# Kernel optimization log

Hardware: AMD Instinct MI355X
Metric: run time of the kernel (lower is better)

The kernel has to match this reference:

```python
import jax, jax.numpy as jnp
import numpy as np

N, E, D, H, C, HOPS = 50000, 1600000, 128, 4, 32, 3

def spectral_normalize(W, iters=5):
    # power iteration, fixed start vector (deterministic, jit-friendly)
    u = jnp.ones((W.shape[0],), W.dtype) / jnp.sqrt(jnp.float32(W.shape[0]))
    for _ in range(iters):
        v = W.T @ u; v = v / (jnp.linalg.norm(v) + 1e-12)
        u = W @ v;  u = u / (jnp.linalg.norm(u) + 1e-12)
    sigma = u @ (W @ v)
    return W / (sigma + 1e-12)

def layer_norm(x, g, b, eps=1e-5):
    m = jnp.mean(x, -1, keepdims=True)
    v = jnp.mean((x - m) ** 2, -1, keepdims=True)
    return (x - m) * jax.lax.rsqrt(v + eps) * g + b

def edge_softmax(logits, dst):
    # logits: [E, H]; softmax over edges sharing a destination node
    m = jax.ops.segment_max(logits, dst, num_segments=N)
    e = jnp.exp(logits - m[dst])
    s = jax.ops.segment_sum(e, dst, num_segments=N)
    return e / (s[dst] + 1e-16)

def gat_layer(h, src, dst, W, a_s, a_d, bias):
    xh = (h @ W).reshape(N, H, C)                      # [N,H,C]
    al_s = jnp.sum(xh * a_s, -1)                       # [N,H]
    al_d = jnp.sum(xh * a_d, -1)
    logits = jax.nn.leaky_relu(al_s[src] + al_d[dst], 0.2)  # [E,H]
    alpha = edge_softmax(logits, dst)                  # [E,H]
    msg = xh[src] * alpha[..., None]                   # [E,H,C]
    out = jax.ops.segment_sum(msg, dst, num_segments=N)
    return out.reshape(N, H * C) + bias

def ode_block(h, W_ode, b_ode, steps=4):
    # fixed-step RK4 over t in [0,1]; f(h) = gelu(h @ sn(W) + b)
    Wn = spectral_normalize(W_ode)
    f = lambda y: jax.nn.gelu(y @ Wn + b_ode, approximate=False)
    dt = 1.0 / steps
    def step(y, _):
        k1 = f(y); k2 = f(y + 0.5 * dt * k1)
        k3 = f(y + 0.5 * dt * k2); k4 = f(y + dt * k3)
        return y + (dt / 6.0) * (k1 + 2 * k2 + 2 * k3 + k4), None
    y, _ = jax.lax.scan(step, h, None, length=steps)
    return y

def multihop_broadcast(h, src, dst, att):
    deg = jnp.maximum(jax.ops.segment_sum(jnp.ones((E,), h.dtype), dst, num_segments=N), 1.0)
    hops = [h]
    cur = h
    for _ in range(HOPS):
        cur = jax.ops.segment_sum(cur[src], dst, num_segments=N) / deg[:, None]
        hops.append(cur)
    stack = jnp.stack(hops)                            # [HOPS+1, N, D]
    scores = jnp.einsum('knd,d->kn', stack, att)       # [HOPS+1, N]
    w = jax.nn.softmax(scores, axis=0)
    return jnp.einsum('kn,knd->nd', w, stack)

def encoder_fwd(x, edge_index, W_in, b_in, W1, a_src1, a_dst1, b1,
                W2, a_src2, a_dst2, b2, g1, be1, g2, be2, W_ode, b_ode, att):
    src, dst = edge_index[0], edge_index[1]
    h = jax.nn.gelu(x @ spectral_normalize(W_in) + b_in, approximate=False)
    h = layer_norm(jax.nn.gelu(gat_layer(h, src, dst, W1, a_src1, a_dst1, b1), approximate=False), g1, be1)
    h = layer_norm(jax.nn.gelu(gat_layer(h, src, dst, W2, a_src2, a_dst2, b2), approximate=False), g2, be2)
    h = ode_block(h, W_ode, b_ode)
    h = multihop_broadcast(h, src, dst, att)
    return h

def setup_inputs() -> dict:
    key = jax.random.key(0)
    ks = jax.random.split(key, 12)
    s = lambda d: 1.0 / np.sqrt(d)
    return {
        'x': jax.random.normal(ks[0], (N, D), jnp.float32),
        'edge_index': jax.random.randint(ks[1], (2, E), 0, N, jnp.int64),
        'W_in': jax.random.normal(ks[2], (D, D), jnp.float32) * s(D),
        'b_in': jnp.zeros((D,), jnp.float32),
        'W1': jax.random.normal(ks[3], (D, H * C), jnp.float32) * s(D),
        'a_src1': jax.random.normal(ks[4], (H, C), jnp.float32) * s(C),
        'a_dst1': jax.random.normal(ks[5], (H, C), jnp.float32) * s(C),
        'b1': jnp.zeros((H * C,), jnp.float32),
        'W2': jax.random.normal(ks[6], (D, H * C), jnp.float32) * s(D),
        'a_src2': jax.random.normal(ks[7], (H, C), jnp.float32) * s(C),
        'a_dst2': jax.random.normal(ks[8], (H, C), jnp.float32) * s(C),
        'b2': jnp.zeros((H * C,), jnp.float32),
        'g1': jnp.ones((D,), jnp.float32), 'be1': jnp.zeros((D,), jnp.float32),
        'g2': jnp.ones((D,), jnp.float32), 'be2': jnp.zeros((D,), jnp.float32),
        'W_ode': jax.random.normal(ks[9], (D, D), jnp.float32) * s(D),
        'b_ode': jnp.zeros((D,), jnp.float32),
        'att': jax.random.normal(ks[10], (D,), jnp.float32) * s(D),
    }

def reference(x, edge_index, W_in, b_in, W1, a_src1, a_dst1, b1, W2, a_src2, a_dst2, b2,
              g1, be1, g2, be2, W_ode, b_ode, att):
    return encoder_fwd(x, edge_index, W_in, b_in, W1, a_src1, a_dst1, b1,
                       W2, a_src2, a_dst2, b2, g1, be1, g2, be2, W_ode, b_ode, att)
```

## Files before the change

kernel.cpp:

```cpp
#include <hip/hip_runtime.h>
#include <math.h>


typedef __attribute__((ext_vector_type(8))) short bf16x8;
typedef __attribute__((ext_vector_type(4))) float f32x4;

__device__ __forceinline__ float gelu_f(float x) {
    return 0.5f * x * (1.0f + erff(x * 0.70710678118654752f));
}
__device__ __forceinline__ unsigned pack_bf16(float a, float b) {
    unsigned ua = __float_as_uint(a), ub = __float_as_uint(b);
    ua += 0x7fffu + ((ua >> 16) & 1u);
    ub += 0x7fffu + ((ub >> 16) & 1u);
    return (ua >> 16) | (ub & 0xffff0000u);
}
__device__ __forceinline__ unsigned short bfbits(float x) {
    unsigned u = __float_as_uint(x);
    u += 0x7fffu + ((u >> 16) & 1u);
    return (unsigned short)(u >> 16);
}
__device__ __forceinline__ float bf_lo(unsigned u) { return __uint_as_float(u << 16); }
__device__ __forceinline__ float bf_hi(unsigned u) { return __uint_as_float(u & 0xffff0000u); }
__device__ __forceinline__ int swz(int byte) { return byte ^ (((byte >> 8) & 15) << 4); }

__launch_bounds__(128, 1)
__global__ void sn_k(const float* __restrict__ Win, const float* __restrict__ Wode,
                     float* __restrict__ WnIn, float* __restrict__ WnOde)
{
    __shared__ float Ws[128 * 128];
    __shared__ float Wt[128 * 128];
    __shared__ float red[128];
    const float* W  = (blockIdx.x == 0) ? Win  : Wode;
    float*       Wn = (blockIdx.x == 0) ? WnIn : WnOde;
    const int t = threadIdx.x;

    for (int i = t * 4; i < 16384; i += 512) {
        float4 v = *(const float4*)&W[i];
        *(float4*)&Ws[i] = v;
        int r = i >> 7, c = i & 127;
        Wt[(c + 0) * 128 + r] = v.x;
        Wt[(c + 1) * 128 + r] = v.y;
        Wt[(c + 2) * 128 + r] = v.z;
        Wt[(c + 3) * 128 + r] = v.w;
    }
    __syncthreads();

    float u = 0.088388347648318447f;
    float v = 0.0f;
    for (int it = 0; it < 5; it++) {
        red[t] = u; __syncthreads();
        float vv = 0.f;
        for (int i = 0; i < 128; i++) vv = fmaf(Ws[i * 128 + t], red[i], vv);
        __syncthreads();
        red[t] = vv * vv; __syncthreads();
        for (int s = 64; s > 0; s >>= 1) { if (t < s) red[t] += red[t + s]; __syncthreads(); }
        float nv = sqrtf(red[0]) + 1e-12f;
        v = vv / nv;
        __syncthreads();
        red[t] = v; __syncthreads();
        float uu = 0.f;
        for (int i = 0; i < 128; i++) uu = fmaf(Wt[i * 128 + t], red[i], uu);
        __syncthreads();
        red[t] = uu * uu; __syncthreads();
        for (int s = 64; s > 0; s >>= 1) { if (t < s) red[t] += red[t + s]; __syncthreads(); }
        float nu = sqrtf(red[0]) + 1e-12f;
        u = uu / nu;
        __syncthreads();
    }
    red[t] = v; __syncthreads();
    float wv = 0.f;
    for (int i = 0; i < 128; i++) wv = fmaf(Wt[i * 128 + t], red[i], wv);
    __syncthreads();
    red[t] = u * wv; __syncthreads();
    for (int s = 64; s > 0; s >>= 1) { if (t < s) red[t] += red[t + s]; __syncthreads(); }
    float inv = 1.0f / (red[0] + 1e-12f);
    __syncthreads();
    for (int i = t * 4; i < 16384; i += 512) {
        float4 w = *(const float4*)&Ws[i];
        w.x *= inv; w.y *= inv; w.z *= inv; w.w *= inv;
        *(float4*)&Wn[i] = w;
    }
}

__global__ void hist_k(const int* __restrict__ dst, int* __restrict__ deg, int E, int N)
{
    int e = blockIdx.x * blockDim.x + threadIdx.x;
    if (e < E) {
        int d = dst[e];
        d = (d < 0) ? 0 : (d >= N ? N - 1 : d);
        atomicAdd(&deg[d], 1);
    }
}

__launch_bounds__(1024, 1)
__global__ void scan_k(const int* __restrict__ deg, int* __restrict__ offs, int n)
{
    __shared__ int part[1024];
    const int t = threadIdx.x;
    const int chunk = (n + 1023) >> 10;
    int lo = t * chunk; if (lo > n) lo = n;
    int hi = lo + chunk; if (hi > n) hi = n;
    int s = 0;
    for (int i = lo; i < hi; i++) s += deg[i];
    part[t] = s; __syncthreads();
    for (int d = 1; d < 1024; d <<= 1) {
        int v = (t >= d) ? part[t - d] : 0;
        __syncthreads();
        part[t] += v;
        __syncthreads();
    }
    int run = (t == 0) ? 0 : part[t - 1];
    for (int i = lo; i < hi; i++) { offs[i] = run; run += deg[i]; }
    if (t == 1023) offs[n] = run;
}

__global__ void scatter_k(const int* __restrict__ src, const int* __restrict__ dst,
                          const int* __restrict__ offs, int* __restrict__ cursor,
                          int* __restrict__ col, int E, int N)
{
    int e = blockIdx.x * blockDim.x + threadIdx.x;
    if (e < E) {
        int d = dst[e];
        d = (d < 0) ? 0 : (d >= N ? N - 1 : d);
        int s = src[e];
        s = (s < 0) ? 0 : (s >= N ? N - 1 : s);
        int pos = offs[d] + atomicAdd(&cursor[d], 1);
        col[pos] = s;
    }
}

__launch_bounds__(256, 2)
__global__ void gemm128_k(const float* __restrict__ in, const float* __restrict__ W,
                          const float* __restrict__ bias, float* __restrict__ out_f32,
                          unsigned* __restrict__ out_bf, int nrows, int mode,
                          const float* __restrict__ a_s, const float* __restrict__ a_d,
                          float* __restrict__ als, float* __restrict__ ald)
{
    __shared__ float Ws[128 * 128];
    const int t = threadIdx.x;
    const int n0 = blockIdx.x * 128;

    for (int i = t * 4; i < 16384; i += 1024)
        *(float4*)&Ws[i] = *(const float4*)&W[i];
    __syncthreads();

    const int cg = t & 15, rg = t >> 4;
    const int c0 = cg * 8, r0 = rg * 8;

    const float* xrow[8];
    bool rowok[8];
#pragma unroll
    for (int i = 0; i < 8; i++) {
        int r = n0 + r0 + i;
        rowok[i] = (r < nrows);
        int rc = rowok[i] ? r : (nrows - 1);
        xrow[i] = in + (size_t)rc * 128;
    }

    float acc[8][8];
#pragma unroll
    for (int i = 0; i < 8; i++)
#pragma unroll
        for (int j = 0; j < 8; j++) acc[i][j] = 0.f;

    for (int k = 0; k < 128; k += 4) {
        float4 xv[8];
#pragma unroll
        for (int i = 0; i < 8; i++) xv[i] = *(const float4*)(xrow[i] + k);
#pragma unroll
        for (int kk = 0; kk < 4; kk++) {
            float4 w0 = *(const float4*)&Ws[(k + kk) * 128 + c0];
            float4 w1 = *(const float4*)&Ws[(k + kk) * 128 + c0 + 4];
#pragma unroll
            for (int i = 0; i < 8; i++) {
                float xk = (kk == 0) ? xv[i].x : (kk == 1) ? xv[i].y : (kk == 2) ? xv[i].z : xv[i].w;
                acc[i][0] = fmaf(xk, w0.x, acc[i][0]);
                acc[i][1] = fmaf(xk, w0.y, acc[i][1]);
                acc[i][2] = fmaf(xk, w0.z, acc[i][2]);
                acc[i][3] = fmaf(xk, w0.w, acc[i][3]);
                acc[i][4] = fmaf(xk, w1.x, acc[i][4]);
                acc[i][5] = fmaf(xk, w1.y, acc[i][5]);
                acc[i][6] = fmaf(xk, w1.z, acc[i][6]);
                acc[i][7] = fmaf(xk, w1.w, acc[i][7]);
            }
        }
    }

    if (mode == 0) {
        const int h = cg >> 2, coff = (cg & 3) * 8;
        float ps[8], pd[8];
#pragma unroll
        for (int i = 0; i < 8; i++) {
            float s_ = 0.f, d_ = 0.f;
#pragma unroll
            for (int j = 0; j < 8; j++) {
                s_ = fmaf(acc[i][j], a_s[h * 32 + coff + j], s_);
                d_ = fmaf(acc[i][j], a_d[h * 32 + coff + j], d_);
            }
            ps[i] = s_; pd[i] = d_;
        }
#pragma unroll
        for (int mk = 1; mk < 4; mk <<= 1) {
#pragma unroll
            for (int i = 0; i < 8; i++) {
                ps[i] += __shfl_xor(ps[i], mk);
                pd[i] += __shfl_xor(pd[i], mk);
            }
        }
        if ((cg & 3) == 0) {
#pragma unroll
            for (int i = 0; i < 8; i++) if (rowok[i]) {
                als[(size_t)(n0 + r0 + i) * 4 + h] = ps[i];
                ald[(size_t)(n0 + r0 + i) * 4 + h] = pd[i];
            }
        }
#pragma unroll
        for (int i = 0; i < 8; i++) if (rowok[i]) {
            size_t b = (size_t)(n0 + r0 + i) * 64 + cg * 4;
            uint4 o;
            o.x = pack_bf16(acc[i][0], acc[i][1]);
            o.y = pack_bf16(acc[i][2], acc[i][3]);
            o.z = pack_bf16(acc[i][4], acc[i][5]);
            o.w = pack_bf16(acc[i][6], acc[i][7]);
            *(uint4*)&out_bf[b] = o;
        }
    } else {
#pragma unroll
        for (int i = 0; i < 8; i++) if (rowok[i]) {
            size_t b = (size_t)(n0 + r0 + i) * 128 + c0;
            float o[8];
#pragma unroll
            for (int j = 0; j < 8; j++) o[j] = gelu_f(acc[i][j] + bias[c0 + j]);
            *(float4*)&out_f32[b]     = make_float4(o[0], o[1], o[2], o[3]);
            *(float4*)&out_f32[b + 4] = make_float4(o[4], o[5], o[6], o[7]);
        }
    }
}

__launch_bounds__(256)
__global__ void gat_agg2_k(const unsigned* __restrict__ xhbf, const float* __restrict__ als,
                           const float* __restrict__ ald, const int* __restrict__ col,
                           const int* __restrict__ offs, const float* __restrict__ bias,
                           const float* __restrict__ g, const float* __restrict__ be,
                           float* __restrict__ hout, int nnodes)
{
    __shared__ float alph[4][64][4];
    __shared__ int   scol[4][64];
    const int w = threadIdx.x >> 6;
    const int n = blockIdx.x * 4 + w;
    if (n >= nnodes) return;
    const int lane = threadIdx.x & 63;
    const int e0 = offs[n], e1 = offs[n + 1];
    const float4 aldv = *(const float4*)&ald[(size_t)n * 4];

    float m0 = -1e30f, m1 = -1e30f, m2 = -1e30f, m3 = -1e30f;
    float s0 = 0.f, s1 = 0.f, s2 = 0.f, s3 = 0.f;
    for (int i = e0 + lane; i < e1; i += 64) {
        int sv = col[i];
        float4 av = *(const float4*)&als[(size_t)sv * 4];
        float l0 = av.x + aldv.x; l0 = l0 > 0.f ? l0 : 0.2f * l0;
        float l1 = av.y + aldv.y; l1 = l1 > 0.f ? l1 : 0.2f * l1;
        float l2 = av.z + aldv.z; l2 = l2 > 0.f ? l2 : 0.2f * l2;
        float l3 = av.w + aldv.w; l3 = l3 > 0.f ? l3 : 0.2f * l3;
        float M;
        M = fmaxf(m0, l0); s0 = s0 * __expf(m0 - M) + __expf(l0 - M); m0 = M;
        M = fmaxf(m1, l1); s1 = s1 * __expf(m1 - M) + __expf(l1 - M); m1 = M;
        M = fmaxf(m2, l2); s2 = s2 * __expf(m2 - M) + __expf(l2 - M); m2 = M;
        M = fmaxf(m3, l3); s3 = s3 * __expf(m3 - M) + __expf(l3 - M); m3 = M;
    }
#pragma unroll
    for (int mk = 1; mk < 64; mk <<= 1) {
        float mo, so, M;
        mo = __shfl_xor(m0, mk); so = __shfl_xor(s0, mk);
        M = fmaxf(m0, mo); s0 = s0 * __expf(m0 - M) + so * __expf(mo - M); m0 = M;
        mo = __shfl_xor(m1, mk); so = __shfl_xor(s1, mk);
        M = fmaxf(m1, mo); s1 = s1 * __expf(m1 - M) + so * __expf(mo - M); m1 = M;
        mo = __shfl_xor(m2, mk); so = __shfl_xor(s2, mk);
        M = fmaxf(m2, mo); s2 = s2 * __expf(m2 - M) + so * __expf(mo - M); m2 = M;
        mo = __shfl_xor(m3, mk); so = __shfl_xor(s3, mk);
        M = fmaxf(m3, mo); s3 = s3 * __expf(m3 - M) + so * __expf(mo - M); m3 = M;
    }
    const float i0 = 1.f / (s0 + 1e-16f), i1 = 1.f / (s1 + 1e-16f);
    const float i2 = 1.f / (s2 + 1e-16f), i3 = 1.f / (s3 + 1e-16f);

    const int hh = lane >> 4;
    float ax = 0.f, ay = 0.f;
    for (int base = e0; base < e1; base += 64) {
        int idx = base + lane;
        if (idx < e1) {
            int sv = col[idx];
            float4 av = *(const float4*)&als[(size_t)sv * 4];
            float l0 = av.x + aldv.x; l0 = l0 > 0.f ? l0 : 0.2f * l0;
            float l1 = av.y + aldv.y; l1 = l1 > 0.f ? l1 : 0.2f * l1;
            float l2 = av.z + aldv.z; l2 = l2 > 0.f ? l2 : 0.2f * l2;
            float l3 = av.w + aldv.w; l3 = l3 > 0.f ? l3 : 0.2f * l3;
            float4 a4;
            a4.x = __expf(l0 - m0) * i0;
            a4.y = __expf(l1 - m1) * i1;
            a4.z = __expf(l2 - m2) * i2;
            a4.w = __expf(l3 - m3) * i3;
            *(float4*)&alph[w][lane][0] = a4;
            scol[w][lane] = sv;
        }
        int cnt = e1 - base; if (cnt > 64) cnt = 64;
#pragma unroll 4
        for (int j = 0; j < cnt; j++) {
            int sj = scol[w][j];
            float aj = alph[w][j][hh];
            unsigned u = xhbf[(size_t)sj * 64 + lane];
            ax = fmaf(aj, bf_lo(u), ax);
            ay = fmaf(aj, bf_hi(u), ay);
        }
    }

    const int c0 = lane * 2;
    float v0 = gelu_f(ax + bias[c0]);
    float v1 = gelu_f(ay + bias[c0 + 1]);
    float sum = v0 + v1;
#pragma unroll
    for (int mk = 32; mk >= 1; mk >>= 1) sum += __shfl_xor(sum, mk);
    float mean = sum * (1.0f / 128.0f);
    float d0 = v0 - mean, d1 = v1 - mean;
    float vs = d0 * d0 + d1 * d1;
#pragma unroll
    for (int mk = 32; mk >= 1; mk >>= 1) vs += __shfl_xor(vs, mk);
    float rstd = rsqrtf(vs * (1.0f / 128.0f) + 1e-5f);
    size_t b = (size_t)n * 128 + c0;
    hout[b]     = d0 * rstd * g[c0] + be[c0];
    hout[b + 1] = d1 * rstd * g[c0 + 1] + be[c0 + 1];
}

__launch_bounds__(256, 4)
__global__ void ode_mfma_k(const float* __restrict__ yin, const float* __restrict__ Wn,
                           const float* __restrict__ bias, unsigned short* __restrict__ ybf,
                           int nrows, int nchunks)
{
    __shared__ unsigned short Wt[128 * 128];
    __shared__ unsigned short tl[2][16 * 128];
    const int t = threadIdx.x;
    const int w = t >> 6, lane = t & 63;
    const int pair = w >> 1, hf = w & 1;
    const int cl = lane & 15, lg = lane >> 4;

    for (int i = t; i < 16384; i += 256) {
        int k = i >> 7, c = i & 127;
        *(unsigned short*)((char*)Wt + swz((c << 8) + (k << 1))) = bfbits(Wn[i]);
    }

    float bcol[4];
#pragma unroll
    for (int n = 0; n < 4; n++) bcol[n] = bias[(hf * 4 + n) * 16 + cl];

    const float dt = 0.25f;
    char* tbase = (char*)&tl[pair][0];

    int chunk = blockIdx.x * 2 + pair;
    if (chunk > nchunks - 1) chunk = nchunks - 1;
    const int r0 = chunk * 16;

    for (int i2 = hf * 64 + lane; i2 < 512; i2 += 128) {
        int r = i2 >> 5, k0 = (i2 & 31) * 4;
        int rc = r0 + r; if (rc > nrows - 1) rc = nrows - 1;
        float4 v = *(const float4*)&yin[(size_t)rc * 128 + k0];
        *(uint2*)(tbase + swz(r * 256 + k0 * 2)) =
            make_uint2(pack_bf16(v.x, v.y), pack_bf16(v.z, v.w));
    }
    float yv[4][4], av[4][4];
#pragma unroll
    for (int q = 0; q < 4; q++) {
        int rc = r0 + lg * 4 + q; if (rc > nrows - 1) rc = nrows - 1;
        const float* rp = &yin[(size_t)rc * 128 + hf * 64 + cl];
#pragma unroll
        for (int n = 0; n < 4; n++) { yv[n][q] = rp[n * 16]; av[n][q] = yv[n][q]; }
    }
    __syncthreads();

#pragma unroll 1
    for (int step = 0; step < 4; step++) {
#pragma unroll 1
        for (int st = 0; st < 4; st++) {
            const float ca = (st == 0 || st == 3) ? dt / 6.f : dt / 3.f;
            const float ct = (st < 2) ? dt * 0.5f : dt;
            const bool last = (st == 3);
            bf16x8 af[4];
#pragma unroll
            for (int ks = 0; ks < 4; ks++)
                af[ks] = *(const bf16x8*)(tbase + swz(cl * 256 + ks * 64 + lg * 16));
            f32x4 acc[4];
#pragma unroll
            for (int n = 0; n < 4; n++) {
                acc[n] = (f32x4){0.f, 0.f, 0.f, 0.f};
#pragma unroll
                for (int ks = 0; ks < 4; ks++) {
                    bf16x8 bf = *(const bf16x8*)((char*)Wt +
                                  swz(((hf * 4 + n) * 16 + cl) * 256 + ks * 64 + lg * 16));
                    acc[n] = __builtin_amdgcn_mfma_f32_16x16x32_bf16(af[ks], bf, acc[n], 0, 0, 0);
                }
            }
            __syncthreads();
#pragma unroll
            for (int n = 0; n < 4; n++) {
#pragma unroll
                for (int q = 0; q < 4; q++) {
                    float kk = gelu_f(acc[n][q] + bcol[n]);
                    av[n][q] = fmaf(ca, kk, av[n][q]);
                    float tn;
                    if (last) { yv[n][q] = av[n][q]; tn = av[n][q]; }
                    else      { tn = fmaf(ct, kk, yv[n][q]); }
                    int rr = lg * 4 + q;
                    *(unsigned short*)(tbase +
                        swz(rr * 256 + ((hf * 4 + n) * 16 + cl) * 2)) = bfbits(tn);
                }
            }
            __syncthreads();
        }
    }
#pragma unroll
    for (int q = 0; q < 4; q++) {
        int rg = r0 + lg * 4 + q;
        if (rg < nrows) {
#pragma unroll
            for (int n = 0; n < 4; n++)
                ybf[(size_t)rg * 128 + hf * 64 + n * 16 + cl] = bfbits(av[n][q]);
        }
    }
}

__launch_bounds__(256)
__global__ void hop_k(const unsigned* __restrict__ cur, const int* __restrict__ col,
                      const int* __restrict__ offs, const int* __restrict__ deg,
                      unsigned* __restrict__ outbf, int nnodes)
{
    __shared__ int scol[4][64];
    const int w = threadIdx.x >> 6;
    const int n = blockIdx.x * 4 + w;
    if (n >= nnodes) return;
    const int lane = threadIdx.x & 63;
    const int e0 = offs[n], e1 = offs[n + 1];
    float ax = 0.f, ay = 0.f;
    for (int base = e0; base < e1; base += 64) {
        int idx = base + lane;
        if (idx < e1) scol[w][lane] = col[idx];
        int cnt = e1 - base; if (cnt > 64) cnt = 64;
#pragma unroll 4
        for (int j = 0; j < cnt; j++) {
            int sj = scol[w][j];
            unsigned u = cur[(size_t)sj * 64 + lane];
            ax += bf_lo(u); ay += bf_hi(u);
        }
    }
    float dg = fmaxf((float)deg[n], 1.0f);
    outbf[(size_t)n * 64 + lane] = pack_bf16(ax / dg, ay / dg);
}

__launch_bounds__(256)
__global__ void final2_k(const unsigned* __restrict__ s0b, const unsigned* __restrict__ s1b,
                         const unsigned* __restrict__ s2b, const unsigned* __restrict__ s3b,
                         const float* __restrict__ att, float* __restrict__ outp, int nnodes)
{
    const int n = blockIdx.x * 4 + (threadIdx.x >> 6);
    if (n >= nnodes) return;
    const int lane = threadIdx.x & 63;
    size_t b = (size_t)n * 64 + lane;
    float2 a = *(const float2*)&att[lane * 2];
    unsigned u0 = s0b[b], u1 = s1b[b], u2 = s2b[b], u3 = s3b[b];
    float p0 = bf_lo(u0) * a.x + bf_hi(u0) * a.y;
    float p1 = bf_lo(u1) * a.x + bf_hi(u1) * a.y;
    float p2 = bf_lo(u2) * a.x + bf_hi(u2) * a.y;
    float p3 = bf_lo(u3) * a.x + bf_hi(u3) * a.y;
#pragma unroll
    for (int mk = 32; mk >= 1; mk >>= 1) {
        p0 += __shfl_xor(p0, mk); p1 += __shfl_xor(p1, mk);
        p2 += __shfl_xor(p2, mk); p3 += __shfl_xor(p3, mk);
    }
    float mm = fmaxf(fmaxf(p0, p1), fmaxf(p2, p3));
    float e0 = __expf(p0 - mm), e1 = __expf(p1 - mm), e2 = __expf(p2 - mm), e3 = __expf(p3 - mm);
    float inv = 1.0f / (e0 + e1 + e2 + e3);
    float w0 = e0 * inv, w1 = e1 * inv, w2 = e2 * inv, w3 = e3 * inv;
    float ox = w0 * bf_lo(u0) + w1 * bf_lo(u1) + w2 * bf_lo(u2) + w3 * bf_lo(u3);
    float oy = w0 * bf_hi(u0) + w1 * bf_hi(u1) + w2 * bf_hi(u2) + w3 * bf_hi(u3);
    *(float2*)&outp[(size_t)n * 128 + lane * 2] = make_float2(ox, oy);
}

extern "C" void kernel_launch(void* const* d_in, const int* in_sizes, int n_in,
                              void* d_out, int out_size, void* d_ws, size_t ws_size,
                              hipStream_t stream)
{
    const float* x     = (const float*)d_in[0];
    const int*   ei    = (const int*)d_in[1];
    const float* W_in  = (const float*)d_in[2];
    const float* b_in  = (const float*)d_in[3];
    const float* W1    = (const float*)d_in[4];
    const float* a_s1  = (const float*)d_in[5];
    const float* a_d1  = (const float*)d_in[6];
    const float* b1    = (const float*)d_in[7];
    const float* W2    = (const float*)d_in[8];
    const float* a_s2  = (const float*)d_in[9];
    const float* a_d2  = (const float*)d_in[10];
    const float* b2    = (const float*)d_in[11];
    const float* g1    = (const float*)d_in[12];
    const float* be1   = (const float*)d_in[13];
    const float* g2    = (const float*)d_in[14];
    const float* be2   = (const float*)d_in[15];
    const float* W_ode = (const float*)d_in[16];
    const float* b_ode = (const float*)d_in[17];
    const float* att   = (const float*)d_in[18];

    const int N = in_sizes[0] / 128;
    const int E = in_sizes[1] / 2;
    const int* srcv = ei;
    const int* dstv = ei + E;

    char* wsb = (char*)d_ws;
    size_t off = 0;
    auto alloc = [&](size_t bytes) -> void* {
        void* p = wsb + off;
        off = (off + bytes + 511) & ~(size_t)511;
        return p;
    };
    float*    WnIn   = (float*)alloc(65536);
    float*    WnOde  = (float*)alloc(65536);
    float*    als    = (float*)alloc((size_t)N * 4 * 4);
    float*    ald    = (float*)alloc((size_t)N * 4 * 4);
    int*      deg    = (int*)alloc((size_t)N * 4);
    int*      cursor = (int*)alloc((size_t)N * 4);
    int*      offs   = (int*)alloc((size_t)(N + 1) * 4);
    int*      col    = (int*)alloc((size_t)E * 4);
    float*    B0     = (float*)alloc((size_t)N * 128 * 4);
    unsigned* xhbf   = (unsigned*)alloc((size_t)N * 64 * 4);
    unsigned* ybf    = (unsigned*)alloc((size_t)N * 64 * 4);
    unsigned* h2bf   = (unsigned*)alloc((size_t)N * 64 * 4);
    unsigned* h3bf   = (unsigned*)alloc((size_t)N * 64 * 4);

    (void)hipMemsetAsync(deg, 0, (size_t)N * 4, stream);
    (void)hipMemsetAsync(cursor, 0, (size_t)N * 4, stream);

    sn_k<<<2, 128, 0, stream>>>(W_in, W_ode, WnIn, WnOde);
    hist_k<<<(E + 255) / 256, 256, 0, stream>>>(dstv, deg, E, N);
    scan_k<<<1, 1024, 0, stream>>>(deg, offs, N);
    scatter_k<<<(E + 255) / 256, 256, 0, stream>>>(srcv, dstv, offs, cursor, col, E, N);

    const int gblocks = (N + 127) / 128;
    const int ablocks = (N + 3) / 4;

    gemm128_k<<<gblocks, 256, 0, stream>>>(x, WnIn, b_in, B0, nullptr, N, 1,
        nullptr, nullptr, nullptr, nullptr);

    gemm128_k<<<gblocks, 256, 0, stream>>>(B0, W1, nullptr, nullptr, xhbf, N, 0,
        a_s1, a_d1, als, ald);
    gat_agg2_k<<<ablocks, 256, 0, stream>>>(xhbf, als, ald, col, offs, b1, g1, be1, B0, N);

    gemm128_k<<<gblocks, 256, 0, stream>>>(B0, W2, nullptr, nullptr, xhbf, N, 0,
        a_s2, a_d2, als, ald);
    gat_agg2_k<<<ablocks, 256, 0, stream>>>(xhbf, als, ald, col, offs, b2, g2, be2, B0, N);

    const int nchunks = (N + 15) / 16;
    const int oblocks = (nchunks + 1) / 2;
    ode_mfma_k<<<oblocks, 256, 0, stream>>>(B0, WnOde, b_ode, (unsigned short*)ybf, N, nchunks);

    hop_k<<<ablocks, 256, 0, stream>>>(ybf,  col, offs, deg, xhbf, N);
    hop_k<<<ablocks, 256, 0, stream>>>(xhbf, col, offs, deg, h2bf, N);
    hop_k<<<ablocks, 256, 0, stream>>>(h2bf, col, offs, deg, h3bf, N);
    final2_k<<<ablocks, 256, 0, stream>>>(ybf, xhbf, h2bf, h3bf, att, (float*)d_out, N);
}
```

Before: 787.2 us.

## Use bf16 MFMA for dense GEMMs and two-pass bucketed CSR scatter

Replaces the fp32 FMA register-tiled GEMM with a bf16 MFMA kernel that stages the input tile and the transposed weights in swizzled LDS, keeping the attention-logit reduction and gelu epilogues. It also replaces the per-edge global-atomic CSR scatter with a two-pass scheme: edges are first bucketed by 256-node destination ranges through LDS into a pair buffer, then each bucket is placed with LDS atomics. The aim is to cut ALU time in the GEMMs and global atomic contention in CSR construction. The cost is lower precision for the fp32 input and hidden activations (now rounded to bf16 before the GEMM), an extra kernel launch, and reuse of the ybf buffer as scratch space. Output stores in the MFMA GEMM are 2-byte scalar writes and may coalesce less well than the previous vector stores.

```diff
diff --git a/kernel.cpp b/kernel.cpp
--- a/kernel.cpp
+++ b/kernel.cpp
@@ -4,6 +4,8 @@
 
 typedef __attribute__((ext_vector_type(8))) short bf16x8;
 typedef __attribute__((ext_vector_type(4))) float f32x4;
+
+#define BSN 256
 
 __device__ __forceinline__ float gelu_f(float x) {
     return 0.5f * x * (1.0f + erff(x * 0.70710678118654752f));
@@ -114,126 +116,201 @@
     if (t == 1023) offs[n] = run;
 }
 
-__global__ void scatter_k(const int* __restrict__ src, const int* __restrict__ dst,
-                          const int* __restrict__ offs, int* __restrict__ cursor,
-                          int* __restrict__ col, int E, int N)
-{
-    int e = blockIdx.x * blockDim.x + threadIdx.x;
-    if (e < E) {
-        int d = dst[e];
-        d = (d < 0) ? 0 : (d >= N ? N - 1 : d);
-        int s = src[e];
-        s = (s < 0) ? 0 : (s >= N ? N - 1 : s);
-        int pos = offs[d] + atomicAdd(&cursor[d], 1);
-        col[pos] = s;
+__global__ void binit_k(const int* __restrict__ offs, int* __restrict__ bcur, int N, int nb)
+{
+    int b = blockIdx.x * blockDim.x + threadIdx.x;
+    if (b < nb) {
+        int n = b * BSN; if (n > N) n = N;
+        bcur[b] = offs[n];
     }
 }
 
 __launch_bounds__(256, 2)
-__global__ void gemm128_k(const float* __restrict__ in, const float* __restrict__ W,
-                          const float* __restrict__ bias, float* __restrict__ out_f32,
-                          unsigned* __restrict__ out_bf, int nrows, int mode,
-                          const float* __restrict__ a_s, const float* __restrict__ a_d,
-                          float* __restrict__ als, float* __restrict__ ald)
-{
-    __shared__ float Ws[128 * 128];
+__global__ void scatA_k(const int* __restrict__ src, const int* __restrict__ dst,
+                        int* __restrict__ bcur, uint2* __restrict__ pairbuf, int E, int N)
+{
+    __shared__ int cnt[256];
+    __shared__ int sc[256];
+    __shared__ int ebase[256];
+    __shared__ int delta[256];
+    __shared__ uint2 pr[4096];
+    __shared__ unsigned char bid[4096];
     const int t = threadIdx.x;
-    const int n0 = blockIdx.x * 128;
-
-    for (int i = t * 4; i < 16384; i += 1024)
-        *(float4*)&Ws[i] = *(const float4*)&W[i];
-    __syncthreads();
-
-    const int cg = t & 15, rg = t >> 4;
-    const int c0 = cg * 8, r0 = rg * 8;
-
-    const float* xrow[8];
-    bool rowok[8];
-#pragma unroll
-    for (int i = 0; i < 8; i++) {
-        int r = n0 + r0 + i;
-        rowok[i] = (r < nrows);
-        int rc = rowok[i] ? r : (nrows - 1);
-        xrow[i] = in + (size_t)rc * 128;
-    }
-
-    float acc[8][8];
-#pragma unroll
-    for (int i = 0; i < 8; i++)
-#pragma unroll
-        for (int j = 0; j < 8; j++) acc[i][j] = 0.f;
-
-    for (int k = 0; k < 128; k += 4) {
-        float4 xv[8];
-#pragma unroll
-        for (int i = 0; i < 8; i++) xv[i] = *(const float4*)(xrow[i] + k);
-#pragma unroll
-        for (int kk = 0; kk < 4; kk++) {
-            float4 w0 = *(const float4*)&Ws[(k + kk) * 128 + c0];
-            float4 w1 = *(const float4*)&Ws[(k + kk) * 128 + c0 + 4];
-#pragma unroll
-            for (int i = 0; i < 8; i++) {
-                float xk = (kk == 0) ? xv[i].x : (kk == 1) ? xv[i].y : (kk == 2) ? xv[i].z : xv[i].w;
-                acc[i][0] = fmaf(xk, w0.x, acc[i][0]);
-                acc[i][1] = fmaf(xk, w0.y, acc[i][1]);
-                acc[i][2] = fmaf(xk, w0.z, acc[i][2]);
-                acc[i][3] = fmaf(xk, w0.w, acc[i][3]);
-                acc[i][4] = fmaf(xk, w1.x, acc[i][4]);
-                acc[i][5] = fmaf(xk, w1.y, acc[i][5]);
-                acc[i][6] = fmaf(xk, w1.z, acc[i][6]);
-                acc[i][7] = fmaf(xk, w1.w, acc[i][7]);
+    const int e0 = blockIdx.x * 4096;
+
+    int s[16], d[16], rk[16], bb[16];
+    cnt[t] = 0;
+    __syncthreads();
+#pragma unroll
+    for (int i = 0; i < 16; i++) {
+        int e = e0 + i * 256 + t;
+        if (e < E) {
+            int dd = dst[e]; dd = (dd < 0) ? 0 : (dd >= N ? N - 1 : dd);
+            int ss = src[e]; ss = (ss < 0) ? 0 : (ss >= N ? N - 1 : ss);
+            s[i] = ss; d[i] = dd; bb[i] = dd >> 8;
+            rk[i] = atomicAdd(&cnt[bb[i]], 1);
+        } else bb[i] = -1;
+    }
+    __syncthreads();
+    sc[t] = cnt[t]; __syncthreads();
+    for (int st = 1; st < 256; st <<= 1) {
+        int v = (t >= st) ? sc[t - st] : 0;
+        __syncthreads();
+        sc[t] += v;
+        __syncthreads();
+    }
+    int excl = sc[t] - cnt[t];
+    int gbase = (cnt[t] > 0) ? atomicAdd(&bcur[t], cnt[t]) : 0;
+    ebase[t] = excl;
+    delta[t] = gbase - excl;
+    __syncthreads();
+#pragma unroll
+    for (int i = 0; i < 16; i++) {
+        if (bb[i] >= 0) {
+            int slot = ebase[bb[i]] + rk[i];
+            pr[slot] = make_uint2((unsigned)s[i], (unsigned)d[i]);
+            bid[slot] = (unsigned char)bb[i];
+        }
+    }
+    __syncthreads();
+    const int total = sc[255];
+    for (int i2 = t; i2 < total; i2 += 256) {
+        int b = bid[i2];
+        pairbuf[delta[b] + i2] = pr[i2];
+    }
+}
+
+__launch_bounds__(256, 4)
+__global__ void scatB_k(const uint2* __restrict__ pairbuf, const int* __restrict__ offs,
+                        int* __restrict__ col, int N)
+{
+    __shared__ int cur[BSN];
+    const int b = blockIdx.x;
+    const int n0 = b * BSN;
+    const int t = threadIdx.x;
+    int nn = N - n0; if (nn > BSN) nn = BSN;
+    if (t < nn) cur[t] = offs[n0 + t];
+    __syncthreads();
+    const int es = offs[n0], ee = offs[n0 + nn];
+    for (int e = es + t; e < ee; e += 256) {
+        uint2 p = pairbuf[e];
+        int pos = atomicAdd(&cur[(int)p.y - n0], 1);
+        col[pos] = (int)p.x;
+    }
+}
+
+__launch_bounds__(256, 2)
+__global__ void gemm_mfma_k(const float* __restrict__ in, const float* __restrict__ W,
+                            const float* __restrict__ bias, float* __restrict__ out_f32,
+                            unsigned short* __restrict__ out_bf, int nrows, int mode,
+                            const float* __restrict__ a_s, const float* __restrict__ a_d,
+                            float* __restrict__ als, float* __restrict__ ald)
+{
+    __shared__ unsigned short Wt[128 * 128];
+    __shared__ unsigned short As[128 * 128];
+    const int t = threadIdx.x;
+    const int w = t >> 6, lane = t & 63;
+    const int cl = lane & 15, lg = lane >> 4;
+    const int r0 = blockIdx.x * 128;
+
+    for (int i = t; i < 16384; i += 256) {
+        int k = i >> 7, c = i & 127;
+        *(unsigned short*)((char*)Wt + swz((c << 8) + (k << 1))) = bfbits(W[i]);
+    }
+    for (int i2 = t; i2 < 4096; i2 += 256) {
+        int r = i2 >> 5, k0 = (i2 & 31) * 4;
+        int rc = r0 + r; if (rc > nrows - 1) rc = nrows - 1;
+        float4 v = *(const float4*)&in[(size_t)rc * 128 + k0];
+        *(uint2*)((char*)As + swz((r << 8) + (k0 << 1))) =
+            make_uint2(pack_bf16(v.x, v.y), pack_bf16(v.z, v.w));
+    }
+    __syncthreads();
+
+    bf16x8 af[2][4];
+#pragma unroll
+    for (int rt = 0; rt < 2; rt++)
+#pragma unroll
+        for (int ks = 0; ks < 4; ks++)
+            af[rt][ks] = *(const bf16x8*)((char*)As +
+                           swz((w * 32 + rt * 16 + cl) * 256 + ks * 64 + lg * 16));
+
+    f32x4 acc[2][8];
+#pragma unroll
+    for (int rt = 0; rt < 2; rt++)
+#pragma unroll
+        for (int n = 0; n < 8; n++) acc[rt][n] = (f32x4){0.f, 0.f, 0.f, 0.f};
+
+#pragma unroll
+    for (int n = 0; n < 8; n++) {
+#pragma unroll
+        for (int ks = 0; ks < 4; ks++) {
+            bf16x8 bf = *(const bf16x8*)((char*)Wt +
+                          swz((n * 16 + cl) * 256 + ks * 64 + lg * 16));
+            acc[0][n] = __builtin_amdgcn_mfma_f32_16x16x32_bf16(af[0][ks], bf, acc[0][n], 0, 0, 0);
+            acc[1][n] = __builtin_amdgcn_mfma_f32_16x16x32_bf16(af[1][ks], bf, acc[1][n], 0, 0, 0);
+        }
+    }
+
+    if (mode == 0) {
+        float asv[4][2], adv[4][2];
+#pragma unroll
+        for (int h = 0; h < 4; h++) {
+            asv[h][0] = a_s[h * 32 + cl];      asv[h][1] = a_s[h * 32 + 16 + cl];
+            adv[h][0] = a_d[h * 32 + cl];      adv[h][1] = a_d[h * 32 + 16 + cl];
+        }
+#pragma unroll
+        for (int rt = 0; rt < 2; rt++) {
+#pragma unroll
+            for (int q = 0; q < 4; q++) {
+                int row = r0 + w * 32 + rt * 16 + lg * 4 + q;
+                float sh[4], dh[4];
+#pragma unroll
+                for (int h = 0; h < 4; h++) {
+                    sh[h] = acc[rt][2 * h][q] * asv[h][0] + acc[rt][2 * h + 1][q] * asv[h][1];
+                    dh[h] = acc[rt][2 * h][q] * adv[h][0] + acc[rt][2 * h + 1][q] * adv[h][1];
+                }
+#pragma unroll
+                for (int mk = 1; mk < 16; mk <<= 1) {
+#pragma unroll
+                    for (int h = 0; h < 4; h++) {
+                        sh[h] += __shfl_xor(sh[h], mk);
+                        dh[h] += __shfl_xor(dh[h], mk);
+                    }
+                }
+                if (cl == 0 && row < nrows) {
+#pragma unroll
+                    for (int h = 0; h < 4; h++) {
+                        als[(size_t)row * 4 + h] = sh[h];
+                        ald[(size_t)row * 4 + h] = dh[h];
+                    }
+                }
             }
-        }
-    }
-
-    if (mode == 0) {
-        const int h = cg >> 2, coff = (cg & 3) * 8;
-        float ps[8], pd[8];
-#pragma unroll
-        for (int i = 0; i < 8; i++) {
-            float s_ = 0.f, d_ = 0.f;
-#pragma unroll
-            for (int j = 0; j < 8; j++) {
-                s_ = fmaf(acc[i][j], a_s[h * 32 + coff + j], s_);
-                d_ = fmaf(acc[i][j], a_d[h * 32 + coff + j], d_);
+#pragma unroll
+            for (int q = 0; q < 4; q++) {
+                int row = r0 + w * 32 + rt * 16 + lg * 4 + q;
+                if (row < nrows) {
+#pragma unroll
+                    for (int n = 0; n < 8; n++)
+                        out_bf[(size_t)row * 128 + n * 16 + cl] = bfbits(acc[rt][n][q]);
+                }
             }
-            ps[i] = s_; pd[i] = d_;
-        }
-#pragma unroll
-        for (int mk = 1; mk < 4; mk <<= 1) {
-#pragma unroll
-            for (int i = 0; i < 8; i++) {
-                ps[i] += __shfl_xor(ps[i], mk);
-                pd[i] += __shfl_xor(pd[i], mk);
+        }
+    } else {
+        float bc[8];
+#pragma unroll
+        for (int n = 0; n < 8; n++) bc[n] = bias[n * 16 + cl];
+#pragma unroll
+        for (int rt = 0; rt < 2; rt++)
+#pragma unroll
+            for (int q = 0; q < 4; q++) {
+                int row = r0 + w * 32 + rt * 16 + lg * 4 + q;
+                if (row < nrows) {
+#pragma unroll
+                    for (int n = 0; n < 8; n++)
+                        out_f32[(size_t)row * 128 + n * 16 + cl] =
+                            gelu_f(acc[rt][n][q] + bc[n]);
+                }
             }
-        }
-        if ((cg & 3) == 0) {
-#pragma unroll
-            for (int i = 0; i < 8; i++) if (rowok[i]) {
-                als[(size_t)(n0 + r0 + i) * 4 + h] = ps[i];
-                ald[(size_t)(n0 + r0 + i) * 4 + h] = pd[i];
-            }
-        }
-#pragma unroll
-        for (int i = 0; i < 8; i++) if (rowok[i]) {
-            size_t b = (size_t)(n0 + r0 + i) * 64 + cg * 4;
-            uint4 o;
-            o.x = pack_bf16(acc[i][0], acc[i][1]);
-            o.y = pack_bf16(acc[i][2], acc[i][3]);
-            o.z = pack_bf16(acc[i][4], acc[i][5]);
-            o.w = pack_bf16(acc[i][6], acc[i][7]);
-            *(uint4*)&out_bf[b] = o;
-        }
-    } else {
-#pragma unroll
-        for (int i = 0; i < 8; i++) if (rowok[i]) {
-            size_t b = (size_t)(n0 + r0 + i) * 128 + c0;
-            float o[8];
-#pragma unroll
-            for (int j = 0; j < 8; j++) o[j] = gelu_f(acc[i][j] + bias[c0 + j]);
-            *(float4*)&out_f32[b]     = make_float4(o[0], o[1], o[2], o[3]);
-            *(float4*)&out_f32[b + 4] = make_float4(o[4], o[5], o[6], o[7]);
-        }
     }
 }
 
@@ -510,6 +587,7 @@
     const int E = in_sizes[1] / 2;
     const int* srcv = ei;
     const int* dstv = ei + E;
+    const int nb = (N + BSN - 1) / BSN;
 
     char* wsb = (char*)d_ws;
     size_t off = 0;
@@ -523,7 +601,7 @@
     float*    als    = (float*)alloc((size_t)N * 4 * 4);
     float*    ald    = (float*)alloc((size_t)N * 4 * 4);
     int*      deg    = (int*)alloc((size_t)N * 4);
-    int*      cursor = (int*)alloc((size_t)N * 4);
+    int*      bcur   = (int*)alloc((size_t)(nb + 1) * 4);
     int*      offs   = (int*)alloc((size_t)(N + 1) * 4);
     int*      col    = (int*)alloc((size_t)E * 4);
     float*    B0     = (float*)alloc((size_t)N * 128 * 4);
@@ -531,27 +609,29 @@
     unsigned* ybf    = (unsigned*)alloc((size_t)N * 64 * 4);
     unsigned* h2bf   = (unsigned*)alloc((size_t)N * 64 * 4);
     unsigned* h3bf   = (unsigned*)alloc((size_t)N * 64 * 4);
+    uint2*    pairbuf = (uint2*)ybf;
 
     (void)hipMemsetAsync(deg, 0, (size_t)N * 4, stream);
-    (void)hipMemsetAsync(cursor, 0, (size_t)N * 4, stream);
 
     sn_k<<<2, 128, 0, stream>>>(W_in, W_ode, WnIn, WnOde);
     hist_k<<<(E + 255) / 256, 256, 0, stream>>>(dstv, deg, E, N);
     scan_k<<<1, 1024, 0, stream>>>(deg, offs, N);
-    scatter_k<<<(E + 255) / 256, 256, 0, stream>>>(srcv, dstv, offs, cursor, col, E, N);
+    binit_k<<<(nb + 255) / 256, 256, 0, stream>>>(offs, bcur, N, nb);
+    scatA_k<<<(E + 4095) / 4096, 256, 0, stream>>>(srcv, dstv, bcur, pairbuf, E, N);
+    scatB_k<<<nb, 256, 0, stream>>>(pairbuf, offs, col, N);
 
     const int gblocks = (N + 127) / 128;
     const int ablocks = (N + 3) / 4;
 
-    gemm128_k<<<gblocks, 256, 0, stream>>>(x, WnIn, b_in, B0, nullptr, N, 1,
+    gemm_mfma_k<<<gblocks, 256, 0, stream>>>(x, WnIn, b_in, B0, nullptr, N, 1,
         nullptr, nullptr, nullptr, nullptr);
 
-    gemm128_k<<<gblocks, 256, 0, stream>>>(B0, W1, nullptr, nullptr, xhbf, N, 0,
-        a_s1, a_d1, als, ald);
+    gemm_mfma_k<<<gblocks, 256, 0, stream>>>(B0, W1, nullptr, nullptr,
+        (unsigned short*)xhbf, N, 0, a_s1, a_d1, als, ald);
     gat_agg2_k<<<ablocks, 256, 0, stream>>>(xhbf, als, ald, col, offs, b1, g1, be1, B0, N);
 
-    gemm128_k<<<gblocks, 256, 0, stream>>>(B0, W2, nullptr, nullptr, xhbf, N, 0,
-        a_s2, a_d2, als, ald);
+    gemm_mfma_k<<<gblocks, 256, 0, stream>>>(B0, W2, nullptr, nullptr,
+        (unsigned short*)xhbf, N, 0, a_s2, a_d2, als, ald);
     gat_agg2_k<<<ablocks, 256, 0, stream>>>(xhbf, als, ald, col, offs, b2, g2, be2, B0, N);
 
     const int nchunks = (N + 15) / 16;
```

Measured after the change: 681.7 us. 13.4% less time.
